# Kernel tuning notes

Hardware: AMD Instinct MI355X
Metric: run time of the kernel (lower is better)

The kernel has to match this reference:

```python
import jax, jax.numpy as jnp
import numpy as np

B, N, E, DIN, DH = 32, 2000, 64000, 128, 128


def setup_inputs() -> dict:
    key = jax.random.key(0)
    ks = jax.random.split(key, 8)
    gene_emb = jax.random.normal(ks[0], (B, N, DIN), dtype=jnp.float32)
    edge_src = jax.random.randint(ks[1], (E,), 0, N, dtype=jnp.int32)
    edge_dst = jax.random.randint(ks[2], (E,), 0, N, dtype=jnp.int32)
    s1 = 1.0 / np.sqrt(DIN)
    s2 = 1.0 / np.sqrt(DH)
    W1 = jax.random.normal(ks[3], (DIN, DH), dtype=jnp.float32) * s1
    b1 = jnp.zeros((DH,), dtype=jnp.float32)
    W2 = jax.random.normal(ks[4], (DH, DH), dtype=jnp.float32) * s2
    b2 = jnp.zeros((DH,), dtype=jnp.float32)
    return {"gene_emb": gene_emb, "edge_src": edge_src, "edge_dst": edge_dst,
            "W1": W1, "b1": b1, "W2": W2, "b2": b2, "pathway_idx": 0}


def _gcn_conv(x, src, dst, norm_e, self_norm, W, b):
    # x: [B, N, Din] -> [B, N, Dout]; PyG GCNConv: linear first, then normalized aggregation
    h = jnp.einsum('bnd,de->bne', x, W)
    msgs = h[:, src, :] * norm_e[None, :, None]          # [B, E, Dout] gather
    agg = jax.vmap(lambda m: jax.ops.segment_sum(m, dst, num_segments=h.shape[1]))(msgs)
    # self-loop contribution (A+I): norm = dinv[i]^2
    return agg + h * self_norm[None, :, None] + b


def reference(gene_emb, edge_src, edge_dst, W1, b1, W2, b2, pathway_idx):
    n = gene_emb.shape[1]
    # symmetric GCN normalization with self loops: deg[i] = in_degree + 1
    deg = jnp.zeros((n,), dtype=gene_emb.dtype).at[edge_dst].add(1.0) + 1.0
    dinv = jax.lax.rsqrt(deg)
    norm_e = dinv[edge_src] * dinv[edge_dst]
    self_norm = dinv * dinv
    x = jax.nn.relu(_gcn_conv(gene_emb, edge_src, edge_dst, norm_e, self_norm, W1, b1))
    x = _gcn_conv(x, edge_src, edge_dst, norm_e, self_norm, W2, b2)
    # global_mean_pool over each graph copy (all graphs have n nodes)
    return jnp.mean(x, axis=1)  # [B, DH]
```

## Files before the change

kernel.cpp:

```cpp
#include <hip/hip_runtime.h>

namespace {
constexpr int NB = 32;
constexpr int NN = 2000;
constexpr int NE = 64000;
constexpr int ND = 128;
constexpr int TR = 32;
constexpr int NCHUNK = (NN + TR - 1) / TR;
constexpr int NXCD = 8;
constexpr int BPB = 2;
constexpr int PAIRS = NB / (NXCD * BPB);
constexpr int GRID_FUSED = NXCD * PAIRS * NCHUNK;
constexpr int SL = 80;
constexpr int ECAP = 1536;

constexpr int CVT_BLOCKS  = 8000;
constexpr int W_BLOCKS    = 8;
constexpr int EDGE_BLOCKS = 250;

constexpr size_t OFF_CNT  = 0;
constexpr size_t OFF_WSUM = OFF_CNT + 2048 * 4;
constexpr size_t OFF_SLOT = OFF_WSUM + 2048 * 4;
constexpr size_t OFF_WF   = OFF_SLOT + (size_t)NN * SL * 4;
constexpr size_t OFF_XBF  = OFF_WF + 32768;
constexpr size_t OFF_YP   = OFF_XBF + (size_t)NB * NN * ND * 2;
constexpr size_t MEMSET_BYTES = 2048 * 4 * 2;

typedef __attribute__((ext_vector_type(8))) short bf16x8;
typedef __attribute__((ext_vector_type(4))) float f32x4;

__device__ __forceinline__ ushort f32_to_bf16(float f) {
    uint u = __float_as_uint(f);
    u += 0x7fffu + ((u >> 16) & 1u);
    return (ushort)(u >> 16);
}
__device__ __forceinline__ uint pack_bf16x2(float lo, float hi) {
    return (uint)f32_to_bf16(lo) | ((uint)f32_to_bf16(hi) << 16);
}
}

__global__ void k_fill(const float* __restrict__ X, ushort* __restrict__ xbf,
                       const float* __restrict__ W1, uint* __restrict__ wf,
                       const int* __restrict__ src, const int* __restrict__ dst,
                       int* __restrict__ cnt, int* __restrict__ slot) {
    const int blk = blockIdx.x;
    if (blk < CVT_BLOCKS) {
        int i = blk * 256 + threadIdx.x;
        float4 v = ((const float4*)X)[i];
        ushort4 o;
        o.x = f32_to_bf16(v.x);
        o.y = f32_to_bf16(v.y);
        o.z = f32_to_bf16(v.z);
        o.w = f32_to_bf16(v.w);
        ((ushort4*)xbf)[i] = o;
    } else if (blk < CVT_BLOCKS + W_BLOCKS) {
        int g = (blk - CVT_BLOCKS) * 256 + threadIdx.x;
        int lane = g & 63, f = g >> 6;
        int nt = f >> 2, kc = f & 3;
        int col = nt * 16 + (lane & 15);
        int k0  = kc * 32 + (lane >> 4) * 8;
        uint4 o;
        o.x = pack_bf16x2(W1[(k0 + 0) * ND + col], W1[(k0 + 1) * ND + col]);
        o.y = pack_bf16x2(W1[(k0 + 2) * ND + col], W1[(k0 + 3) * ND + col]);
        o.z = pack_bf16x2(W1[(k0 + 4) * ND + col], W1[(k0 + 5) * ND + col]);
        o.w = pack_bf16x2(W1[(k0 + 6) * ND + col], W1[(k0 + 7) * ND + col]);
        ((uint4*)wf)[g] = o;
    } else {
        int e = (blk - CVT_BLOCKS - W_BLOCKS) * 256 + threadIdx.x;
        int s = src[e], d = dst[e];
        int p = atomicAdd(&cnt[d], 1);
        if (p < SL) slot[d * SL + p] = s;
    }
}

__global__ void k_wsum(const int* __restrict__ src, const int* __restrict__ dst,
                       const int* __restrict__ cnt, float* __restrict__ wsum) {
    int e = blockIdx.x * 256 + threadIdx.x;
    if (e < NE) {
        int s = src[e], d = dst[e];
        float w = rsqrtf((float)(cnt[s] + 1)) * rsqrtf((float)(cnt[d] + 1));
        atomicAdd(&wsum[s], w);
    }
}

__global__ __launch_bounds__(256, 4) void k_fused(const ushort* __restrict__ xbf,
                                                  const int* __restrict__ cnt,
                                                  const int* __restrict__ slot,
                                                  const float* __restrict__ wsum,
                                                  const uint* __restrict__ wfrag,
                                                  const float* __restrict__ b1,
                                                  float* __restrict__ ypart) {
    __shared__ uint  AsU[2][32 * 68];
    __shared__ int2  sEdge[ECAP];
    __shared__ int   sCnt[32];
    __shared__ int   sBase[33];
    __shared__ float sDinv[32];
    __shared__ float sWn[32];
    __shared__ float yred[2][128];
    const int tid = threadIdx.x;

    const int L     = blockIdx.x;
    const int xcd   = L & (NXCD - 1);
    const int sl    = L >> 3;
    const int pair  = sl / NCHUNK;
    const int chunk = sl % NCHUNK;
    const int b0    = xcd * (BPB * PAIRS) + pair * BPB;
    const int n0    = chunk * TR;

    if (tid < 32) {
        int n = n0 + tid;
        int cr = (n < NN) ? cnt[n] : 0;
        float d = rsqrtf((float)(cr + 1));
        sCnt[tid]  = min(cr, SL);
        sDinv[tid] = d;
        sWn[tid]   = (n < NN) ? (wsum[n] + d * d) : 0.f;
    }
    if (tid < 128) { yred[0][tid] = 0.f; yred[1][tid] = 0.f; }
    __syncthreads();
    if (tid == 0) {
        int s = 0;
        for (int j = 0; j < 32; j++) { sBase[j] = s; s += sCnt[j]; }
        sBase[32] = s;
    }
    __syncthreads();
    const bool staged = (sBase[32] <= ECAP);

    const int wv = tid >> 6, ln = tid & 63;
    if (staged) {
        for (int ii = 0; ii < 8; ii++) {
            int j = wv * 8 + ii;
            int c = sCnt[j];
            float dd = sDinv[j];
            const int* sp = &slot[(size_t)(n0 + j) * SL];
            for (int base = 0; base < c; base += 64) {
                if (base + ln < c) {
                    int sidx = sp[base + ln];
                    float w = rsqrtf((float)(cnt[sidx] + 1)) * dd;
                    sEdge[sBase[j] + base + ln] = make_int2(sidx, __float_as_int(w));
                }
            }
        }
    }
    __syncthreads();

    const uint* __restrict__ Xu0 = (const uint*)(xbf + (size_t)b0 * NN * ND);
    const uint* __restrict__ Xu1 = (const uint*)(xbf + (size_t)(b0 + 1) * NN * ND);
    #pragma unroll 1
    for (int ii = 0; ii < 8; ii++) {
        const int j = wv * 8 + ii;
        const int n = n0 + j;
        float2 a0 = make_float2(0.f, 0.f), a1 = a0, a0b = a0, a1b = a0;
        if (n < NN) {
            float sn = sDinv[j]; sn *= sn;
            uint u0 = Xu0[n * 64 + ln], u1 = Xu1[n * 64 + ln];
            a0.x = sn * __uint_as_float(u0 << 16);
            a0.y = sn * __uint_as_float(u0 & 0xffff0000u);
            a1.x = sn * __uint_as_float(u1 << 16);
            a1.y = sn * __uint_as_float(u1 & 0xffff0000u);
            const int c = sCnt[j];
            if (staged) {
                const int e0 = sBase[j], e1 = e0 + c;
                int e = e0;
                for (; e + 8 <= e1; e += 8) {
                    int sidx[8]; float w[8]; uint q0[8], q1[8];
                    #pragma unroll
                    for (int q = 0; q < 8; q++) {
                        int2 ed = sEdge[e + q];
                        sidx[q] = ed.x; w[q] = __int_as_float(ed.y);
                    }
                    #pragma unroll
                    for (int q = 0; q < 8; q++) {
                        q0[q] = Xu0[sidx[q] * 64 + ln];
                        q1[q] = Xu1[sidx[q] * 64 + ln];
                    }
                    #pragma unroll
                    for (int q = 0; q < 8; q++) {
                        float x0l = __uint_as_float(q0[q] << 16);
                        float x0h = __uint_as_float(q0[q] & 0xffff0000u);
                        float x1l = __uint_as_float(q1[q] << 16);
                        float x1h = __uint_as_float(q1[q] & 0xffff0000u);
                        if (q & 1) {
                            a0b.x = fmaf(w[q], x0l, a0b.x);
                            a0b.y = fmaf(w[q], x0h, a0b.y);
                            a1b.x = fmaf(w[q], x1l, a1b.x);
                            a1b.y = fmaf(w[q], x1h, a1b.y);
                        } else {
                            a0.x = fmaf(w[q], x0l, a0.x);
                            a0.y = fmaf(w[q], x0h, a0.y);
                            a1.x = fmaf(w[q], x1l, a1.x);
                            a1.y = fmaf(w[q], x1h, a1.y);
                        }
                    }
                }
                for (; e < e1; e++) {
                    int2 ed = sEdge[e];
                    float w = __int_as_float(ed.y);
                    uint u0e = Xu0[ed.x * 64 + ln], u1e = Xu1[ed.x * 64 + ln];
                    a0.x = fmaf(w, __uint_as_float(u0e << 16), a0.x);
                    a0.y = fmaf(w, __uint_as_float(u0e & 0xffff0000u), a0.y);
                    a1.x = fmaf(w, __uint_as_float(u1e << 16), a1.x);
                    a1.y = fmaf(w, __uint_as_float(u1e & 0xffff0000u), a1.y);
                }
            } else {
                const int* sp = &slot[(size_t)n * SL];
                float dd = sDinv[j];
                for (int e = 0; e < c; e++) {
                    int sidx = sp[e];
                    float w = rsqrtf((float)(cnt[sidx] + 1)) * dd;
                    uint u0e = Xu0[sidx * 64 + ln], u1e = Xu1[sidx * 64 + ln];
                    a0.x = fmaf(w, __uint_as_float(u0e << 16), a0.x);
                    a0.y = fmaf(w, __uint_as_float(u0e & 0xffff0000u), a0.y);
                    a1.x = fmaf(w, __uint_as_float(u1e << 16), a1.x);
                    a1.y = fmaf(w, __uint_as_float(u1e & 0xffff0000u), a1.y);
                }
            }
            a0.x += a0b.x; a0.y += a0b.y;
            a1.x += a1b.x; a1.y += a1b.y;
        }
        AsU[0][j * 68 + ln] = pack_bf16x2(a0.x, a0.y);
        AsU[1][j * 68 + ln] = pack_bf16x2(a1.x, a1.y);
    }
    __syncthreads();

    const int lane15 = ln & 15, quad = ln >> 4;
    f32x4 zero4 = {0.f, 0.f, 0.f, 0.f};
    f32x4 acc[2][2][2];
    #pragma unroll
    for (int b = 0; b < 2; b++)
        #pragma unroll
        for (int mt = 0; mt < 2; mt++)
            #pragma unroll
            for (int nt2 = 0; nt2 < 2; nt2++) acc[b][mt][nt2] = zero4;

    bf16x8 wf[2][4];
    const bf16x8* Wf8 = (const bf16x8*)wfrag;
    #pragma unroll
    for (int nt2 = 0; nt2 < 2; nt2++)
        #pragma unroll
        for (int kc = 0; kc < 4; kc++)
            wf[nt2][kc] = Wf8[(((2 * wv + nt2) * 4 + kc) * 64) + ln];

    const bf16x8* A8_0 = (const bf16x8*)AsU[0];
    const bf16x8* A8_1 = (const bf16x8*)AsU[1];
    #pragma unroll
    for (int mt = 0; mt < 2; mt++) {
        const int r = mt * 16 + lane15;
        #pragma unroll
        for (int kc = 0; kc < 4; kc++) {
            bf16x8 af0 = A8_0[r * 17 + kc * 4 + quad];
            bf16x8 af1 = A8_1[r * 17 + kc * 4 + quad];
            #pragma unroll
            for (int nt2 = 0; nt2 < 2; nt2++) {
                acc[0][mt][nt2] = __builtin_amdgcn_mfma_f32_16x16x32_bf16(
                    af0, wf[nt2][kc], acc[0][mt][nt2], 0, 0, 0);
                acc[1][mt][nt2] = __builtin_amdgcn_mfma_f32_16x16x32_bf16(
                    af1, wf[nt2][kc], acc[1][mt][nt2], 0, 0, 0);
            }
        }
    }

    #pragma unroll
    for (int nt2 = 0; nt2 < 2; nt2++) {
        int cg = (2 * wv + nt2) * 16 + lane15;
        float bias = b1[cg];
        #pragma unroll
        for (int b = 0; b < 2; b++) {
            float part = 0.f;
            #pragma unroll
            for (int mt = 0; mt < 2; mt++) {
                f32x4 a = acc[b][mt][nt2];
                #pragma unroll
                for (int r = 0; r < 4; r++) {
                    int m = mt * 16 + quad * 4 + r;
                    part = fmaf(sWn[m], fmaxf(a[r] + bias, 0.f), part);
                }
            }
            atomicAdd(&yred[b][cg], part);
        }
    }
    __syncthreads();
    if (tid < 128)
        ypart[((size_t)b0 * NCHUNK + chunk) * ND + tid] = yred[0][tid];
    else
        ypart[((size_t)(b0 + 1) * NCHUNK + chunk) * ND + (tid - 128)] = yred[1][tid - 128];
}

__global__ __launch_bounds__(128) void k_out(const float* __restrict__ ypart,
                                             const float* __restrict__ W2,
                                             const float* __restrict__ b2,
                                             float* __restrict__ out) {
    __shared__ float ys[128];
    const int b = blockIdx.x;
    const int d = threadIdx.x;
    float s = 0.f;
    for (int c = 0; c < NCHUNK; c++)
        s += ypart[((size_t)b * NCHUNK + c) * ND + d];
    ys[d] = s * (1.f / (float)NN);
    __syncthreads();
    float acc = b2[d];
    #pragma unroll 8
    for (int k = 0; k < 128; k++)
        acc = fmaf(ys[k], W2[k * ND + d], acc);
    out[b * ND + d] = acc;
}

extern "C" void kernel_launch(void* const* d_in, const int* in_sizes, int n_in,
                              void* d_out, int out_size, void* d_ws, size_t ws_size,
                              hipStream_t stream) {
    (void)in_sizes; (void)n_in; (void)out_size; (void)ws_size;
    const float* X   = (const float*)d_in[0];
    const int*   src = (const int*)d_in[1];
    const int*   dst = (const int*)d_in[2];
    const float* W1  = (const float*)d_in[3];
    const float* b1  = (const float*)d_in[4];
    const float* W2  = (const float*)d_in[5];
    const float* b2  = (const float*)d_in[6];
    float* out = (float*)d_out;

    char* ws = (char*)d_ws;
    int*    cnt   = (int*)   (ws + OFF_CNT);
    float*  wsum  = (float*) (ws + OFF_WSUM);
    int*    slot  = (int*)   (ws + OFF_SLOT);
    uint*   wfb   = (uint*)  (ws + OFF_WF);
    ushort* xbf   = (ushort*)(ws + OFF_XBF);
    float*  ypart = (float*) (ws + OFF_YP);

    (void)hipMemsetAsync(ws, 0, MEMSET_BYTES, stream);
    k_fill<<<CVT_BLOCKS + W_BLOCKS + EDGE_BLOCKS, 256, 0, stream>>>(
        X, xbf, W1, wfb, src, dst, cnt, slot);
    k_wsum<<<EDGE_BLOCKS, 256, 0, stream>>>(src, dst, cnt, wsum);
    k_fused<<<GRID_FUSED, 256, 0, stream>>>(xbf, cnt, slot, wsum, wfb, b1, ypart);
    k_out<<<NB, 128, 0, stream>>>(ypart, W2, b2, out);
}
```

Before: 165.6 us.

## Precompute edge weights in CSR, halve row tile, fuse output GEMV via ticket

Edge weights are now computed once in the second prep pass and stored alongside source indices, so the fused kernel stages them without per-block rsqrt or prefix sums. The fused kernel uses 16-row tiles with half-wave edge splitting and 8-byte gathers, shuffle reductions, and global atomics into y. The last block per batch pair, found with a ticket counter, does the mean and W2 GEMV, which removes the separate output kernel. Conversion blocks process eight float4 each. The changes add atomic contention and a last-block serial tail in exchange for fewer launches and higher occupancy.

```diff
diff --git a/kernel.cpp b/kernel.cpp
--- a/kernel.cpp
+++ b/kernel.cpp
@@ -5,26 +5,28 @@
 constexpr int NN = 2000;
 constexpr int NE = 64000;
 constexpr int ND = 128;
-constexpr int TR = 32;
-constexpr int NCHUNK = (NN + TR - 1) / TR;
+constexpr int TR = 16;
+constexpr int NCHUNK = NN / TR;
 constexpr int NXCD = 8;
 constexpr int BPB = 2;
-constexpr int PAIRS = NB / (NXCD * BPB);
-constexpr int GRID_FUSED = NXCD * PAIRS * NCHUNK;
+constexpr int PAIRS_PER_XCD = NB / (NXCD * BPB);
+constexpr int NPAIR = NB / BPB;
+constexpr int GRID_FUSED = NPAIR * NCHUNK;
 constexpr int SL = 80;
-constexpr int ECAP = 1536;
-
-constexpr int CVT_BLOCKS  = 8000;
+
+constexpr int CVT_BLOCKS  = 1000;
 constexpr int W_BLOCKS    = 8;
 constexpr int EDGE_BLOCKS = 250;
 
-constexpr size_t OFF_CNT  = 0;
-constexpr size_t OFF_WSUM = OFF_CNT + 2048 * 4;
-constexpr size_t OFF_SLOT = OFF_WSUM + 2048 * 4;
-constexpr size_t OFF_WF   = OFF_SLOT + (size_t)NN * SL * 4;
-constexpr size_t OFF_XBF  = OFF_WF + 32768;
-constexpr size_t OFF_YP   = OFF_XBF + (size_t)NB * NN * ND * 2;
-constexpr size_t MEMSET_BYTES = 2048 * 4 * 2;
+constexpr size_t OFF_CNT    = 0;
+constexpr size_t OFF_CNT2   = 8192;
+constexpr size_t OFF_WSUM   = 16384;
+constexpr size_t OFF_Y      = 24576;
+constexpr size_t OFF_TICKET = 40960;
+constexpr size_t MEMSET_BYTES = 41216;
+constexpr size_t OFF_SLOT2  = 41216;
+constexpr size_t OFF_WF     = OFF_SLOT2 + (size_t)NN * SL * 8;
+constexpr size_t OFF_XBF    = OFF_WF + 32768;
 
 typedef __attribute__((ext_vector_type(8))) short bf16x8;
 typedef __attribute__((ext_vector_type(4))) float f32x4;
@@ -39,20 +41,25 @@
 }
 }
 
-__global__ void k_fill(const float* __restrict__ X, ushort* __restrict__ xbf,
-                       const float* __restrict__ W1, uint* __restrict__ wf,
-                       const int* __restrict__ src, const int* __restrict__ dst,
-                       int* __restrict__ cnt, int* __restrict__ slot) {
+__global__ void k_prep1(const float* __restrict__ X, ushort* __restrict__ xbf,
+                        const float* __restrict__ W1, uint* __restrict__ wf,
+                        const int* __restrict__ dst, int* __restrict__ cnt) {
     const int blk = blockIdx.x;
     if (blk < CVT_BLOCKS) {
-        int i = blk * 256 + threadIdx.x;
-        float4 v = ((const float4*)X)[i];
-        ushort4 o;
-        o.x = f32_to_bf16(v.x);
-        o.y = f32_to_bf16(v.y);
-        o.z = f32_to_bf16(v.z);
-        o.w = f32_to_bf16(v.w);
-        ((ushort4*)xbf)[i] = o;
+        const float4* __restrict__ X4 = (const float4*)X;
+        ushort4* __restrict__ O4 = (ushort4*)xbf;
+        const int base = blk * 2048 + (int)threadIdx.x;
+        #pragma unroll
+        for (int k = 0; k < 8; k++) {
+            int i = base + k * 256;
+            float4 v = X4[i];
+            ushort4 o;
+            o.x = f32_to_bf16(v.x);
+            o.y = f32_to_bf16(v.y);
+            o.z = f32_to_bf16(v.z);
+            o.w = f32_to_bf16(v.w);
+            O4[i] = o;
+        }
     } else if (blk < CVT_BLOCKS + W_BLOCKS) {
         int g = (blk - CVT_BLOCKS) * 256 + threadIdx.x;
         int lane = g & 63, f = g >> 6;
@@ -67,195 +74,185 @@
         ((uint4*)wf)[g] = o;
     } else {
         int e = (blk - CVT_BLOCKS - W_BLOCKS) * 256 + threadIdx.x;
-        int s = src[e], d = dst[e];
-        int p = atomicAdd(&cnt[d], 1);
-        if (p < SL) slot[d * SL + p] = s;
-    }
-}
-
-__global__ void k_wsum(const int* __restrict__ src, const int* __restrict__ dst,
-                       const int* __restrict__ cnt, float* __restrict__ wsum) {
+        atomicAdd(&cnt[dst[e]], 1);
+    }
+}
+
+__global__ void k_prep2(const int* __restrict__ src, const int* __restrict__ dst,
+                        const int* __restrict__ cnt, int* __restrict__ cnt2,
+                        float* __restrict__ wsum, int2* __restrict__ slot2) {
     int e = blockIdx.x * 256 + threadIdx.x;
-    if (e < NE) {
-        int s = src[e], d = dst[e];
-        float w = rsqrtf((float)(cnt[s] + 1)) * rsqrtf((float)(cnt[d] + 1));
-        atomicAdd(&wsum[s], w);
-    }
+    int s = src[e], d = dst[e];
+    float w = rsqrtf((float)(cnt[s] + 1)) * rsqrtf((float)(cnt[d] + 1));
+    int p = atomicAdd(&cnt2[d], 1);
+    if (p < SL) slot2[(size_t)d * SL + p] = make_int2(s, __float_as_int(w));
+    atomicAdd(&wsum[s], w);
 }
 
 __global__ __launch_bounds__(256, 4) void k_fused(const ushort* __restrict__ xbf,
                                                   const int* __restrict__ cnt,
-                                                  const int* __restrict__ slot,
+                                                  const int2* __restrict__ slot2,
                                                   const float* __restrict__ wsum,
                                                   const uint* __restrict__ wfrag,
                                                   const float* __restrict__ b1,
-                                                  float* __restrict__ ypart) {
-    __shared__ uint  AsU[2][32 * 68];
-    __shared__ int2  sEdge[ECAP];
-    __shared__ int   sCnt[32];
-    __shared__ int   sBase[33];
-    __shared__ float sDinv[32];
-    __shared__ float sWn[32];
-    __shared__ float yred[2][128];
+                                                  const float* __restrict__ W2,
+                                                  const float* __restrict__ b2,
+                                                  float* __restrict__ y,
+                                                  int* __restrict__ ticket,
+                                                  float* __restrict__ out) {
+    __shared__ __align__(16) uint AsU[2][TR * 68];
+    __shared__ int2  sE[TR][SL];
+    __shared__ float sDinv[TR];
+    __shared__ float sWn[TR];
+    __shared__ int   sCnt[TR];
+    __shared__ float ysl[2][ND];
+    __shared__ int   sWin;
     const int tid = threadIdx.x;
 
     const int L     = blockIdx.x;
     const int xcd   = L & (NXCD - 1);
     const int sl    = L >> 3;
     const int pair  = sl / NCHUNK;
-    const int chunk = sl % NCHUNK;
-    const int b0    = xcd * (BPB * PAIRS) + pair * BPB;
+    const int chunk = sl - pair * NCHUNK;
+    const int b0    = xcd * (BPB * PAIRS_PER_XCD) + pair * BPB;
+    const int gp    = xcd * PAIRS_PER_XCD + pair;
     const int n0    = chunk * TR;
 
-    if (tid < 32) {
+    if (tid < TR) {
         int n = n0 + tid;
-        int cr = (n < NN) ? cnt[n] : 0;
+        int cr = cnt[n];
         float d = rsqrtf((float)(cr + 1));
         sCnt[tid]  = min(cr, SL);
         sDinv[tid] = d;
-        sWn[tid]   = (n < NN) ? (wsum[n] + d * d) : 0.f;
-    }
-    if (tid < 128) { yred[0][tid] = 0.f; yred[1][tid] = 0.f; }
+        sWn[tid]   = wsum[n] + d * d;
+    }
     __syncthreads();
-    if (tid == 0) {
-        int s = 0;
-        for (int j = 0; j < 32; j++) { sBase[j] = s; s += sCnt[j]; }
-        sBase[32] = s;
-    }
-    __syncthreads();
-    const bool staged = (sBase[32] <= ECAP);
 
     const int wv = tid >> 6, ln = tid & 63;
-    if (staged) {
-        for (int ii = 0; ii < 8; ii++) {
-            int j = wv * 8 + ii;
-            int c = sCnt[j];
-            float dd = sDinv[j];
-            const int* sp = &slot[(size_t)(n0 + j) * SL];
-            for (int base = 0; base < c; base += 64) {
-                if (base + ln < c) {
-                    int sidx = sp[base + ln];
-                    float w = rsqrtf((float)(cnt[sidx] + 1)) * dd;
-                    sEdge[sBase[j] + base + ln] = make_int2(sidx, __float_as_int(w));
+    const int p = ln >> 5, col = ln & 31;
+    const uint2* __restrict__ X0 = (const uint2*)(xbf + (size_t)b0 * NN * ND);
+    const uint2* __restrict__ X1 = X0 + (size_t)NN * ND / 4;
+
+    #pragma unroll
+    for (int ii = 0; ii < 4; ii++) {
+        int j = wv * 4 + ii;
+        int c = sCnt[j];
+        const int2* sp = slot2 + (size_t)(n0 + j) * SL;
+        for (int base = 0; base < c; base += 64)
+            if (base + ln < c) sE[j][base + ln] = sp[base + ln];
+    }
+
+    #pragma unroll 1
+    for (int ii = 0; ii < 4; ii++) {
+        const int j = wv * 4 + ii;
+        const int n = n0 + j;
+        const int c = sCnt[j];
+        float4 a  = {0.f, 0.f, 0.f, 0.f}, ab = a;
+        float4 g  = a, gb = a;
+        {
+            uint2 q = X0[(size_t)p * (NN * ND / 4) + n * 32 + col];
+            float sn = sDinv[j] * sDinv[j];
+            float w0 = p ? 0.f : sn;
+            float w1 = p ? sn : 0.f;
+            float f0 = __uint_as_float(q.x << 16);
+            float f1 = __uint_as_float(q.x & 0xffff0000u);
+            float f2 = __uint_as_float(q.y << 16);
+            float f3 = __uint_as_float(q.y & 0xffff0000u);
+            a.x = w0 * f0; a.y = w0 * f1; a.z = w0 * f2; a.w = w0 * f3;
+            g.x = w1 * f0; g.y = w1 * f1; g.z = w1 * f2; g.w = w1 * f3;
+        }
+        int e = 0;
+        for (; e + 8 <= c; e += 8) {
+            int sidx[4]; float w[4]; uint2 q0[4], q1[4];
+            #pragma unroll
+            for (int q = 0; q < 4; q++) {
+                int2 ed = sE[j][e + 2 * q + p];
+                sidx[q] = ed.x; w[q] = __int_as_float(ed.y);
+            }
+            #pragma unroll
+            for (int q = 0; q < 4; q++) {
+                int off = sidx[q] * 32 + col;
+                q0[q] = X0[off];
+                q1[q] = X1[off];
+            }
+            #pragma unroll
+            for (int q = 0; q < 4; q++) {
+                float f0 = __uint_as_float(q0[q].x << 16);
+                float f1 = __uint_as_float(q0[q].x & 0xffff0000u);
+                float f2 = __uint_as_float(q0[q].y << 16);
+                float f3 = __uint_as_float(q0[q].y & 0xffff0000u);
+                float h0 = __uint_as_float(q1[q].x << 16);
+                float h1 = __uint_as_float(q1[q].x & 0xffff0000u);
+                float h2 = __uint_as_float(q1[q].y << 16);
+                float h3 = __uint_as_float(q1[q].y & 0xffff0000u);
+                if (q & 1) {
+                    ab.x = fmaf(w[q], f0, ab.x); ab.y = fmaf(w[q], f1, ab.y);
+                    ab.z = fmaf(w[q], f2, ab.z); ab.w = fmaf(w[q], f3, ab.w);
+                    gb.x = fmaf(w[q], h0, gb.x); gb.y = fmaf(w[q], h1, gb.y);
+                    gb.z = fmaf(w[q], h2, gb.z); gb.w = fmaf(w[q], h3, gb.w);
+                } else {
+                    a.x = fmaf(w[q], f0, a.x); a.y = fmaf(w[q], f1, a.y);
+                    a.z = fmaf(w[q], f2, a.z); a.w = fmaf(w[q], f3, a.w);
+                    g.x = fmaf(w[q], h0, g.x); g.y = fmaf(w[q], h1, g.y);
+                    g.z = fmaf(w[q], h2, g.z); g.w = fmaf(w[q], h3, g.w);
                 }
             }
         }
-    }
-    __syncthreads();
-
-    const uint* __restrict__ Xu0 = (const uint*)(xbf + (size_t)b0 * NN * ND);
-    const uint* __restrict__ Xu1 = (const uint*)(xbf + (size_t)(b0 + 1) * NN * ND);
-    #pragma unroll 1
-    for (int ii = 0; ii < 8; ii++) {
-        const int j = wv * 8 + ii;
-        const int n = n0 + j;
-        float2 a0 = make_float2(0.f, 0.f), a1 = a0, a0b = a0, a1b = a0;
-        if (n < NN) {
-            float sn = sDinv[j]; sn *= sn;
-            uint u0 = Xu0[n * 64 + ln], u1 = Xu1[n * 64 + ln];
-            a0.x = sn * __uint_as_float(u0 << 16);
-            a0.y = sn * __uint_as_float(u0 & 0xffff0000u);
-            a1.x = sn * __uint_as_float(u1 << 16);
-            a1.y = sn * __uint_as_float(u1 & 0xffff0000u);
-            const int c = sCnt[j];
-            if (staged) {
-                const int e0 = sBase[j], e1 = e0 + c;
-                int e = e0;
-                for (; e + 8 <= e1; e += 8) {
-                    int sidx[8]; float w[8]; uint q0[8], q1[8];
-                    #pragma unroll
-                    for (int q = 0; q < 8; q++) {
-                        int2 ed = sEdge[e + q];
-                        sidx[q] = ed.x; w[q] = __int_as_float(ed.y);
-                    }
-                    #pragma unroll
-                    for (int q = 0; q < 8; q++) {
-                        q0[q] = Xu0[sidx[q] * 64 + ln];
-                        q1[q] = Xu1[sidx[q] * 64 + ln];
-                    }
-                    #pragma unroll
-                    for (int q = 0; q < 8; q++) {
-                        float x0l = __uint_as_float(q0[q] << 16);
-                        float x0h = __uint_as_float(q0[q] & 0xffff0000u);
-                        float x1l = __uint_as_float(q1[q] << 16);
-                        float x1h = __uint_as_float(q1[q] & 0xffff0000u);
-                        if (q & 1) {
-                            a0b.x = fmaf(w[q], x0l, a0b.x);
-                            a0b.y = fmaf(w[q], x0h, a0b.y);
-                            a1b.x = fmaf(w[q], x1l, a1b.x);
-                            a1b.y = fmaf(w[q], x1h, a1b.y);
-                        } else {
-                            a0.x = fmaf(w[q], x0l, a0.x);
-                            a0.y = fmaf(w[q], x0h, a0.y);
-                            a1.x = fmaf(w[q], x1l, a1.x);
-                            a1.y = fmaf(w[q], x1h, a1.y);
-                        }
-                    }
-                }
-                for (; e < e1; e++) {
-                    int2 ed = sEdge[e];
-                    float w = __int_as_float(ed.y);
-                    uint u0e = Xu0[ed.x * 64 + ln], u1e = Xu1[ed.x * 64 + ln];
-                    a0.x = fmaf(w, __uint_as_float(u0e << 16), a0.x);
-                    a0.y = fmaf(w, __uint_as_float(u0e & 0xffff0000u), a0.y);
-                    a1.x = fmaf(w, __uint_as_float(u1e << 16), a1.x);
-                    a1.y = fmaf(w, __uint_as_float(u1e & 0xffff0000u), a1.y);
-                }
-            } else {
-                const int* sp = &slot[(size_t)n * SL];
-                float dd = sDinv[j];
-                for (int e = 0; e < c; e++) {
-                    int sidx = sp[e];
-                    float w = rsqrtf((float)(cnt[sidx] + 1)) * dd;
-                    uint u0e = Xu0[sidx * 64 + ln], u1e = Xu1[sidx * 64 + ln];
-                    a0.x = fmaf(w, __uint_as_float(u0e << 16), a0.x);
-                    a0.y = fmaf(w, __uint_as_float(u0e & 0xffff0000u), a0.y);
-                    a1.x = fmaf(w, __uint_as_float(u1e << 16), a1.x);
-                    a1.y = fmaf(w, __uint_as_float(u1e & 0xffff0000u), a1.y);
-                }
-            }
-            a0.x += a0b.x; a0.y += a0b.y;
-            a1.x += a1b.x; a1.y += a1b.y;
-        }
-        AsU[0][j * 68 + ln] = pack_bf16x2(a0.x, a0.y);
-        AsU[1][j * 68 + ln] = pack_bf16x2(a1.x, a1.y);
+        for (; e < c; e += 2) {
+            int ee = e + p;
+            int eidx = (ee < c) ? ee : e;
+            int2 ed = sE[j][eidx];
+            float w = (ee < c) ? __int_as_float(ed.y) : 0.f;
+            int off = ed.x * 32 + col;
+            uint2 u0 = X0[off], u1 = X1[off];
+            a.x = fmaf(w, __uint_as_float(u0.x << 16), a.x);
+            a.y = fmaf(w, __uint_as_float(u0.x & 0xffff0000u), a.y);
+            a.z = fmaf(w, __uint_as_float(u0.y << 16), a.z);
+            a.w = fmaf(w, __uint_as_float(u0.y & 0xffff0000u), a.w);
+            g.x = fmaf(w, __uint_as_float(u1.x << 16), g.x);
+            g.y = fmaf(w, __uint_as_float(u1.x & 0xffff0000u), g.y);
+            g.z = fmaf(w, __uint_as_float(u1.y << 16), g.z);
+            g.w = fmaf(w, __uint_as_float(u1.y & 0xffff0000u), g.w);
+        }
+        a.x += ab.x; a.y += ab.y; a.z += ab.z; a.w += ab.w;
+        g.x += gb.x; g.y += gb.y; g.z += gb.z; g.w += gb.w;
+        a.x += __shfl_xor(a.x, 32); a.y += __shfl_xor(a.y, 32);
+        a.z += __shfl_xor(a.z, 32); a.w += __shfl_xor(a.w, 32);
+        g.x += __shfl_xor(g.x, 32); g.y += __shfl_xor(g.y, 32);
+        g.z += __shfl_xor(g.z, 32); g.w += __shfl_xor(g.w, 32);
+        float4 av;
+        av.x = p ? g.x : a.x; av.y = p ? g.y : a.y;
+        av.z = p ? g.z : a.z; av.w = p ? g.w : a.w;
+        AsU[p][j * 68 + 2 * col]     = pack_bf16x2(av.x, av.y);
+        AsU[p][j * 68 + 2 * col + 1] = pack_bf16x2(av.z, av.w);
     }
     __syncthreads();
 
     const int lane15 = ln & 15, quad = ln >> 4;
     f32x4 zero4 = {0.f, 0.f, 0.f, 0.f};
-    f32x4 acc[2][2][2];
-    #pragma unroll
-    for (int b = 0; b < 2; b++)
-        #pragma unroll
-        for (int mt = 0; mt < 2; mt++)
-            #pragma unroll
-            for (int nt2 = 0; nt2 < 2; nt2++) acc[b][mt][nt2] = zero4;
-
-    bf16x8 wf[2][4];
+    f32x4 acc[2][2];
+    acc[0][0] = zero4; acc[0][1] = zero4; acc[1][0] = zero4; acc[1][1] = zero4;
+
+    bf16x8 wfv[2][4];
     const bf16x8* Wf8 = (const bf16x8*)wfrag;
     #pragma unroll
     for (int nt2 = 0; nt2 < 2; nt2++)
         #pragma unroll
         for (int kc = 0; kc < 4; kc++)
-            wf[nt2][kc] = Wf8[(((2 * wv + nt2) * 4 + kc) * 64) + ln];
-
-    const bf16x8* A8_0 = (const bf16x8*)AsU[0];
-    const bf16x8* A8_1 = (const bf16x8*)AsU[1];
+            wfv[nt2][kc] = Wf8[(((2 * wv + nt2) * 4 + kc) * 64) + ln];
+
+    const bf16x8* A0 = (const bf16x8*)AsU[0];
+    const bf16x8* A1 = (const bf16x8*)AsU[1];
     #pragma unroll
-    for (int mt = 0; mt < 2; mt++) {
-        const int r = mt * 16 + lane15;
+    for (int kc = 0; kc < 4; kc++) {
+        bf16x8 af0 = A0[lane15 * 17 + kc * 4 + quad];
+        bf16x8 af1 = A1[lane15 * 17 + kc * 4 + quad];
         #pragma unroll
-        for (int kc = 0; kc < 4; kc++) {
-            bf16x8 af0 = A8_0[r * 17 + kc * 4 + quad];
-            bf16x8 af1 = A8_1[r * 17 + kc * 4 + quad];
-            #pragma unroll
-            for (int nt2 = 0; nt2 < 2; nt2++) {
-                acc[0][mt][nt2] = __builtin_amdgcn_mfma_f32_16x16x32_bf16(
-                    af0, wf[nt2][kc], acc[0][mt][nt2], 0, 0, 0);
-                acc[1][mt][nt2] = __builtin_amdgcn_mfma_f32_16x16x32_bf16(
-                    af1, wf[nt2][kc], acc[1][mt][nt2], 0, 0, 0);
-            }
+        for (int nt2 = 0; nt2 < 2; nt2++) {
+            acc[0][nt2] = __builtin_amdgcn_mfma_f32_16x16x32_bf16(
+                af0, wfv[nt2][kc], acc[0][nt2], 0, 0, 0);
+            acc[1][nt2] = __builtin_amdgcn_mfma_f32_16x16x32_bf16(
+                af1, wfv[nt2][kc], acc[1][nt2], 0, 0, 0);
         }
     }
 
@@ -267,41 +264,33 @@
         for (int b = 0; b < 2; b++) {
             float part = 0.f;
             #pragma unroll
-            for (int mt = 0; mt < 2; mt++) {
-                f32x4 a = acc[b][mt][nt2];
-                #pragma unroll
-                for (int r = 0; r < 4; r++) {
-                    int m = mt * 16 + quad * 4 + r;
-                    part = fmaf(sWn[m], fmaxf(a[r] + bias, 0.f), part);
-                }
-            }
-            atomicAdd(&yred[b][cg], part);
-        }
-    }
+            for (int r = 0; r < 4; r++)
+                part = fmaf(sWn[quad * 4 + r], fmaxf(acc[b][nt2][r] + bias, 0.f), part);
+            part += __shfl_xor(part, 16);
+            part += __shfl_xor(part, 32);
+            if (quad == 0) atomicAdd(&y[(b0 + b) * ND + cg], part);
+        }
+    }
+
+    __threadfence();
     __syncthreads();
-    if (tid < 128)
-        ypart[((size_t)b0 * NCHUNK + chunk) * ND + tid] = yred[0][tid];
-    else
-        ypart[((size_t)(b0 + 1) * NCHUNK + chunk) * ND + (tid - 128)] = yred[1][tid - 128];
-}
-
-__global__ __launch_bounds__(128) void k_out(const float* __restrict__ ypart,
-                                             const float* __restrict__ W2,
-                                             const float* __restrict__ b2,
-                                             float* __restrict__ out) {
-    __shared__ float ys[128];
-    const int b = blockIdx.x;
-    const int d = threadIdx.x;
-    float s = 0.f;
-    for (int c = 0; c < NCHUNK; c++)
-        s += ypart[((size_t)b * NCHUNK + c) * ND + d];
-    ys[d] = s * (1.f / (float)NN);
+    if (tid == 0) {
+        int old = atomicAdd(&ticket[gp], 1);
+        sWin = (old == NCHUNK - 1) ? 1 : 0;
+    }
     __syncthreads();
-    float acc = b2[d];
-    #pragma unroll 8
-    for (int k = 0; k < 128; k++)
-        acc = fmaf(ys[k], W2[k * ND + d], acc);
-    out[b * ND + d] = acc;
+    if (sWin) {
+        const int bb = tid >> 7;
+        const int dd = tid & 127;
+        float v = atomicAdd(&y[(b0 + bb) * ND + dd], 0.f);
+        ysl[bb][dd] = v * (1.f / (float)NN);
+        __syncthreads();
+        float acc2 = b2[dd];
+        #pragma unroll 8
+        for (int k = 0; k < ND; k++)
+            acc2 = fmaf(ysl[bb][k], W2[k * ND + dd], acc2);
+        out[(b0 + bb) * ND + dd] = acc2;
+    }
 }
 
 extern "C" void kernel_launch(void* const* d_in, const int* in_sizes, int n_in,
@@ -318,17 +307,19 @@
     float* out = (float*)d_out;
 
     char* ws = (char*)d_ws;
-    int*    cnt   = (int*)   (ws + OFF_CNT);
-    float*  wsum  = (float*) (ws + OFF_WSUM);
-    int*    slot  = (int*)   (ws + OFF_SLOT);
-    uint*   wfb   = (uint*)  (ws + OFF_WF);
-    ushort* xbf   = (ushort*)(ws + OFF_XBF);
-    float*  ypart = (float*) (ws + OFF_YP);
+    int*    cnt    = (int*)   (ws + OFF_CNT);
+    int*    cnt2   = (int*)   (ws + OFF_CNT2);
+    float*  wsum   = (float*) (ws + OFF_WSUM);
+    float*  y      = (float*) (ws + OFF_Y);
+    int*    ticket = (int*)   (ws + OFF_TICKET);
+    int2*   slot2  = (int2*)  (ws + OFF_SLOT2);
+    uint*   wfb    = (uint*)  (ws + OFF_WF);
+    ushort* xbf    = (ushort*)(ws + OFF_XBF);
 
     (void)hipMemsetAsync(ws, 0, MEMSET_BYTES, stream);
-    k_fill<<<CVT_BLOCKS + W_BLOCKS + EDGE_BLOCKS, 256, 0, stream>>>(
-        X, xbf, W1, wfb, src, dst, cnt, slot);
-    k_wsum<<<EDGE_BLOCKS, 256, 0, stream>>>(src, dst, cnt, wsum);
-    k_fused<<<GRID_FUSED, 256, 0, stream>>>(xbf, cnt, slot, wsum, wfb, b1, ypart);
-    k_out<<<NB, 128, 0, stream>>>(ypart, W2, b2, out);
-}
+    k_prep1<<<CVT_BLOCKS + W_BLOCKS + EDGE_BLOCKS, 256, 0, stream>>>(
+        X, xbf, W1, wfb, dst, cnt);
+    k_prep2<<<EDGE_BLOCKS, 256, 0, stream>>>(src, dst, cnt, cnt2, wsum, slot2);
+    k_fused<<<GRID_FUSED, 256, 0, stream>>>(xbf, cnt, slot2, wsum, wfb, b1,
+                                            W2, b2, y, ticket, out);
+}
```

New measurement: 279.6 us. 68.8% more time.
